# Performance work log

Measured on AMD Instinct MI355X. Metric: run time of the kernel, lower is better.

The kernel has to match this reference:

```python
import jax, jax.numpy as jnp
import numpy as np

B, S, D, E = 4, 2048, 2048, 8


def setup_inputs() -> dict:
    key = jax.random.key(0)
    ks = jax.random.split(key, 5)
    scale = 1.0 / np.sqrt(D)
    x = jax.random.normal(ks[0], (B, S, D), dtype=jnp.float32)
    # experts: torch Linear stores W as [out, in]; y = x @ W.T + b
    expert_w = jax.random.uniform(ks[1], (E, D, D), dtype=jnp.float32, minval=-scale, maxval=scale)
    expert_b = jax.random.uniform(ks[2], (E, D), dtype=jnp.float32, minval=-scale, maxval=scale)
    router_w = jax.random.uniform(ks[3], (E, D), dtype=jnp.float32, minval=-scale, maxval=scale)
    router_b = jax.random.uniform(ks[4], (E,), dtype=jnp.float32, minval=-scale, maxval=scale)
    return {"x": x, "expert_w": expert_w, "expert_b": expert_b,
            "router_w": router_w, "router_b": router_b}


def reference(x, expert_w, expert_b, router_w, router_b):
    b, s, d = x.shape
    n_exp = expert_w.shape[0]
    xf = x.reshape(b * s, d)                       # [N, D]
    logits = xf @ router_w.T + router_b            # [N, E]
    probs = jax.nn.softmax(logits, axis=-1)
    expert_id = jnp.argmax(probs, axis=-1)         # [N] top-1 routing
    top_prob = jnp.max(probs, axis=-1)             # [N] gate weight
    out = jnp.zeros_like(xf)
    # dense-equivalent of the masked gather/scatter: each expert's linear
    # applied to all tokens, masked by routing decision (E is small & static)
    for i in range(n_exp):
        y = xf @ expert_w[i].T + expert_b[i]       # [N, D]
        out = out + jnp.where((expert_id == i)[:, None], y, 0.0)
    out = out * top_prob[:, None]
    # forward never calls compute_loss; returns loss = 0
    return out.reshape(b, s, d), jnp.float32(0.0)
```

## Files before the change

### kernel.cpp

```cpp
#include <hip/hip_runtime.h>
#include <hip/hip_bf16.h>

#define N_TOK 8192
#define DIM   2048
#define NEXP  8
#define BM    288
#define BN    256
#define BK    32
#define NT    (DIM / BK)
#define NBLK  256

#define A_BYTES  (BM * BK * 2)
#define B_BYTES  (BN * BK * 2)
#define RING     (A_BYTES + B_BYTES)
#define DYN_LDS  (4 * RING)

typedef __attribute__((ext_vector_type(8))) short  short8;
typedef __attribute__((ext_vector_type(4))) float  f32x4;
typedef __attribute__((ext_vector_type(4))) unsigned int u32x4;

static __device__ __forceinline__ unsigned int pack_bf2(float a, float b) {
  union { __hip_bfloat16 h; unsigned short u; } ca, cb;
  ca.h = __float2bfloat16(a);
  cb.h = __float2bfloat16(b);
  return ((unsigned int)cb.u << 16) | (unsigned int)ca.u;
}

static __device__ __forceinline__ void gload16(const unsigned short* g, void* l) {
  __builtin_amdgcn_global_load_lds(
      (const __attribute__((address_space(1))) unsigned int*)(const void*)g,
      (__attribute__((address_space(3))) unsigned int*)l, 16, 0, 0);
}

static __device__ __forceinline__ double dot8d(const float4& x0, const float4& x1,
                                               const float4& w0, const float4& w1) {
  double a = 0.0;
  a = fma((double)x0.x, (double)w0.x, a);
  a = fma((double)x0.y, (double)w0.y, a);
  a = fma((double)x0.z, (double)w0.z, a);
  a = fma((double)x0.w, (double)w0.w, a);
  a = fma((double)x1.x, (double)w1.x, a);
  a = fma((double)x1.y, (double)w1.y, a);
  a = fma((double)x1.z, (double)w1.z, a);
  a = fma((double)x1.w, (double)w1.w, a);
  return a;
}

__global__ __launch_bounds__(256) void convw_kernel(
    const float* __restrict__ w, unsigned short* __restrict__ wbuf)
{
  const size_t c0 = (size_t)blockIdx.x * 1024 + threadIdx.x;
  float4 f[8];
#pragma unroll
  for (int i = 0; i < 4; i++) {
    const float4* s = reinterpret_cast<const float4*>(w + (c0 + i * 256) * 8);
    f[2 * i]     = s[0];
    f[2 * i + 1] = s[1];
  }
#pragma unroll
  for (int i = 0; i < 4; i++) {
    u32x4 pk;
    pk[0] = pack_bf2(f[2*i].x,   f[2*i].y);   pk[1] = pack_bf2(f[2*i].z,   f[2*i].w);
    pk[2] = pack_bf2(f[2*i+1].x, f[2*i+1].y); pk[3] = pack_bf2(f[2*i+1].z, f[2*i+1].w);
    *reinterpret_cast<u32x4*>(wbuf + (c0 + i * 256) * 8) = pk;
  }
}

__global__ __launch_bounds__(256, 3) void router_kernel(
    const float* __restrict__ x, const float* __restrict__ rw,
    const float* __restrict__ rb, int* __restrict__ eid,
    float* __restrict__ gate, unsigned short* __restrict__ xb)
{
  const int t    = threadIdx.x;
  const int tok0 = blockIdx.x * 4;

  float4 w0[NEXP], w1[NEXP];
#pragma unroll
  for (int e = 0; e < NEXP; e++) {
    const float4* wr = reinterpret_cast<const float4*>(rw + (size_t)e * DIM);
    w0[e] = wr[2 * t];
    w1[e] = wr[2 * t + 1];
  }
  float4 xv0[4], xv1[4];
#pragma unroll
  for (int k = 0; k < 4; k++) {
    const float4* xr = reinterpret_cast<const float4*>(x + (size_t)(tok0 + k) * DIM);
    xv0[k] = xr[2 * t];
    xv1[k] = xr[2 * t + 1];
  }
#pragma unroll
  for (int k = 0; k < 4; k++) {
    u32x4 pk;
    pk[0] = pack_bf2(xv0[k].x, xv0[k].y); pk[1] = pack_bf2(xv0[k].z, xv0[k].w);
    pk[2] = pack_bf2(xv1[k].x, xv1[k].y); pk[3] = pack_bf2(xv1[k].z, xv1[k].w);
    *reinterpret_cast<u32x4*>(xb + (size_t)(tok0 + k) * DIM + t * 8) = pk;
  }

  __shared__ double red[4][4][NEXP];
  const int lane = t & 63, wv = t >> 6;
#pragma unroll
  for (int k = 0; k < 4; k++) {
    double s[NEXP];
#pragma unroll
    for (int e = 0; e < NEXP; e++) s[e] = dot8d(xv0[k], xv1[k], w0[e], w1[e]);
#pragma unroll
    for (int e = 0; e < NEXP; e++) {
      double v = s[e];
#pragma unroll
      for (int off = 32; off > 0; off >>= 1) v += __shfl_xor(v, off, 64);
      if (lane == 0) red[wv][k][e] = v;
    }
  }
  __syncthreads();
  if (t < 4) {
    double lg[NEXP];
    double lmax = -1e300; int best = 0;
#pragma unroll
    for (int e = 0; e < NEXP; e++) {
      lg[e] = red[0][t][e] + red[1][t][e] + red[2][t][e] + red[3][t][e] + (double)rb[e];
      if (lg[e] > lmax) { lmax = lg[e]; best = e; }
    }
    float den = 0.f;
#pragma unroll
    for (int e = 0; e < NEXP; e++) den += expf((float)(lg[e] - lmax));
    eid[tok0 + t]  = best;
    gate[tok0 + t] = 1.0f / den;
  }
}

__global__ __launch_bounds__(1024) void histo_perm(
    const int* __restrict__ eid, int* __restrict__ counts, int* __restrict__ perm)
{
  __shared__ int hist[NEXP], baseS[NEXP], fillS[NEXP];
  const int t = threadIdx.x;
  if (t < NEXP) { hist[t] = 0; fillS[t] = 0; }
  __syncthreads();
  int my[8];
#pragma unroll
  for (int i = 0; i < 8; i++) {
    my[i] = eid[t + i * 1024];
    atomicAdd(&hist[my[i]], 1);
  }
  __syncthreads();
  if (t == 0) {
    int b = 0;
#pragma unroll
    for (int e = 0; e < NEXP; e++) { counts[e] = hist[e]; baseS[e] = b; b += hist[e]; }
  }
  __syncthreads();
#pragma unroll
  for (int i = 0; i < 8; i++) {
    int pos = baseS[my[i]] + atomicAdd(&fillS[my[i]], 1);
    perm[pos] = t + i * 1024;
  }
}

__global__ __launch_bounds__(512, 2) void moe_gemm(
    const unsigned short* __restrict__ xb, const unsigned short* __restrict__ wb,
    const float* __restrict__ eb, const float* __restrict__ gate,
    const int* __restrict__ perm, const int* __restrict__ counts,
    float* __restrict__ out)
{
  extern __shared__ char smem[];
  __shared__ int   aRowS[BM];
  __shared__ float gateS[BM];

  const int tid  = threadIdx.x;
  const int lane = tid & 63, wid = tid >> 6;

  int ttot = 0;
#pragma unroll
  for (int j = 0; j < NEXP; j++) ttot += (counts[j] + BM - 1) / BM;
  ttot *= 8;
  const int tq = ttot >> 3, tr = ttot & 7;

  const int nA5 = (wid < 2);
  int aR0[3], bR0[2];
  aR0[0] = (wid * 2) * 16;
  aR0[1] = (wid * 2 + 1) * 16;
  aR0[2] = nA5 ? ((16 + wid) * 16) : aR0[0];
  bR0[0] = (wid * 2) * 16;
  bR0[1] = (wid * 2 + 1) * 16;
  int aDst[3], bDst[2];
#pragma unroll
  for (int i = 0; i < 3; i++) aDst[i] = aR0[i] * 64;
#pragma unroll
  for (int i = 0; i < 2; i++) bDst[i] = A_BYTES + bR0[i] * 64;
  const int lrow = lane >> 2;
  const int cblk = (lane & 3) ^ ((lane >> 3) & 3);

  const int l15 = lane & 15;
  const int wr = wid >> 2, wc = wid & 3;
  const int sw   = (((lane >> 4) ^ ((l15 >> 1) & 3)) * 16);
  const int aOff = (wr * 144 + l15) * 64 + sw;
  const int bOff = A_BYTES + (wc * 64 + l15) * 64 + sw;
  const int rsub = (lane >> 4) * 4;

  for (int ti = blockIdx.x; ti < ttot; ti += NBLK) {
    const int k  = ti & 7, j = ti >> 3;
    const int tt = k * tq + (k < tr ? k : tr) + j;
    const int bx = tt >> 3, by = tt & 7;

    int e = 0, rowbase = 0, nrows = 0, found = 0;
    {
      int tsum = 0, bsum = 0;
#pragma unroll
      for (int jj = 0; jj < NEXP; jj++) {
        int cj = counts[jj];
        int te = (cj + BM - 1) / BM;
        if (!found && bx < tsum + te) {
          int loc = bx - tsum;
          e = jj;
          rowbase = bsum + loc * BM;
          int rem = cj - loc * BM;
          nrows = rem < BM ? rem : BM;
          found = 1;
        }
        tsum += te; bsum += cj;
      }
    }

    __syncthreads();
    if (tid < BM) {
      int idx = tid < nrows ? tid : (nrows - 1);
      int tok = perm[rowbase + idx];
      aRowS[tid] = tok;
      gateS[tid] = gate[tok];
    }
    __syncthreads();

    const unsigned short* wB = wb + (size_t)e * DIM * DIM;
    const unsigned short* aSrc[3];
    const unsigned short* bSrc[2];
#pragma unroll
    for (int i = 0; i < 3; i++)
      aSrc[i] = xb + (size_t)aRowS[aR0[i] + lrow] * DIM + cblk * 8;
#pragma unroll
    for (int i = 0; i < 2; i++)
      bSrc[i] = wB + (size_t)(by * BN + bR0[i] + lrow) * DIM + cblk * 8;

#pragma unroll
    for (int p = 0; p < 3; p++) {
      char* base = smem + p * RING;
      gload16(aSrc[0], base + aDst[0]);
      gload16(aSrc[1], base + aDst[1]);
      if (nA5) gload16(aSrc[2], base + aDst[2]);
      gload16(bSrc[0], base + bDst[0]);
      gload16(bSrc[1], base + bDst[1]);
      aSrc[0] += BK; aSrc[1] += BK; aSrc[2] += BK;
      bSrc[0] += BK; bSrc[1] += BK;
    }

    f32x4 acc[9][4] = {};

#pragma unroll 1
    for (int t = 0; t < NT; ++t) {
      if (t < NT - 2) {
        if (nA5) asm volatile("s_waitcnt vmcnt(10)" ::: "memory");
        else     asm volatile("s_waitcnt vmcnt(8)"  ::: "memory");
      } else if (t == NT - 2) {
        if (nA5) asm volatile("s_waitcnt vmcnt(5)" ::: "memory");
        else     asm volatile("s_waitcnt vmcnt(4)" ::: "memory");
      } else {
        asm volatile("s_waitcnt vmcnt(0)" ::: "memory");
      }
      __builtin_amdgcn_s_barrier();

      if (t + 3 < NT) {
        char* base = smem + ((t + 3) & 3) * RING;
        gload16(aSrc[0], base + aDst[0]);
        gload16(aSrc[1], base + aDst[1]);
        if (nA5) gload16(aSrc[2], base + aDst[2]);
        gload16(bSrc[0], base + bDst[0]);
        gload16(bSrc[1], base + bDst[1]);
        aSrc[0] += BK; aSrc[1] += BK; aSrc[2] += BK;
        bSrc[0] += BK; bSrc[1] += BK;
      }

      const char* cur = smem + (t & 3) * RING;
      short8 af[9], bf[4];
#pragma unroll
      for (int n = 0; n < 4; n++) bf[n] = *(const short8*)(cur + bOff + n * 1024);
#pragma unroll
      for (int m = 0; m < 9; m++) af[m] = *(const short8*)(cur + aOff + m * 1024);
      __builtin_amdgcn_s_setprio(1);
#pragma unroll
      for (int m = 0; m < 9; m++)
#pragma unroll
        for (int n = 0; n < 4; n++)
          acc[m][n] = __builtin_amdgcn_mfma_f32_16x16x32_bf16(af[m], bf[n], acc[m][n], 0, 0, 0);
      __builtin_amdgcn_s_setprio(0);
    }

    const int cb = by * BN + wc * 64;
    const float* ebE = eb + (size_t)e * DIM;
    float bias[4];
#pragma unroll
    for (int n = 0; n < 4; n++) bias[n] = ebE[cb + n * 16 + l15];
#pragma unroll
    for (int m = 0; m < 9; m++) {
      int r0 = wr * 144 + m * 16 + rsub;
#pragma unroll
      for (int rg = 0; rg < 4; rg++) {
        int r = r0 + rg;
        if (r < nrows) {
          float g = gateS[r];
          float* orow = out + (size_t)aRowS[r] * DIM + cb;
#pragma unroll
          for (int n = 0; n < 4; n++)
            orow[n * 16 + l15] = (acc[m][n][rg] + bias[n]) * g;
        }
      }
    }
    asm volatile("s_waitcnt vmcnt(0)" ::: "memory");
  }
}

extern "C" void kernel_launch(void* const* d_in, const int* in_sizes, int n_in,
                              void* d_out, int out_size, void* d_ws, size_t ws_size,
                              hipStream_t stream)
{
  const float* x  = (const float*)d_in[0];
  const float* ew = (const float*)d_in[1];
  const float* eb = (const float*)d_in[2];
  const float* rw = (const float*)d_in[3];
  const float* rb = (const float*)d_in[4];
  float* out = (float*)d_out;

  char* ws = (char*)d_ws;
  int*   eid    = (int*)(ws);
  float* gate   = (float*)(ws + 32 * 1024);
  int*   counts = (int*)(ws + 64 * 1024);
  int*   perm   = (int*)(ws + 128 * 1024);
  unsigned short* xbuf = (unsigned short*)(ws + 192 * 1024);
  unsigned short* wbuf = (unsigned short*)(ws + 192 * 1024 + ((size_t)N_TOK * DIM * 2));

  hipFuncSetAttribute(reinterpret_cast<const void*>(moe_gemm),
                      hipFuncAttributeMaxDynamicSharedMemorySize, DYN_LDS);

  hipMemsetAsync(out + (size_t)N_TOK * DIM, 0, sizeof(float), stream);
  convw_kernel<<<4096, 256, 0, stream>>>(ew, wbuf);
  router_kernel<<<N_TOK / 4, 256, 0, stream>>>(x, rw, rb, eid, gate, xbuf);
  histo_perm<<<1, 1024, 0, stream>>>(eid, counts, perm);
  moe_gemm<<<NBLK, 512, DYN_LDS, stream>>>(xbuf, wbuf, eb, gate, perm, counts, out);
}
```

Baseline: 173.1 us.

## Fuse fp32-to-bf16 weight conversion into MoE GEMM B-tile loads

Drops the separate weight conversion kernel and has the GEMM load fp32 expert weights straight into LDS, converting them to bf16 in registers before the MFMAs. This removes a full pass that reads 128MB of fp32 weights and writes bf16 copies. In exchange, B-tile traffic from global memory doubles (fp32), the LDS ring shrinks from 4 to 3 stages, and each k-step adds pack/convert ALU work. Each weight tile is also re-read by many row tiles, so the fp32 reads repeat across blocks.

```diff
diff --git a/kernel.cpp b/kernel.cpp
--- a/kernel.cpp
+++ b/kernel.cpp
@@ -11,9 +11,9 @@
 #define NBLK  256
 
 #define A_BYTES  (BM * BK * 2)
-#define B_BYTES  (BN * BK * 2)
+#define B_BYTES  (BN * BK * 4)
 #define RING     (A_BYTES + B_BYTES)
-#define DYN_LDS  (4 * RING)
+#define DYN_LDS  (3 * RING)
 
 typedef __attribute__((ext_vector_type(8))) short  short8;
 typedef __attribute__((ext_vector_type(4))) float  f32x4;
@@ -26,9 +26,9 @@
   return ((unsigned int)cb.u << 16) | (unsigned int)ca.u;
 }
 
-static __device__ __forceinline__ void gload16(const unsigned short* g, void* l) {
+static __device__ __forceinline__ void gload16(const void* g, void* l) {
   __builtin_amdgcn_global_load_lds(
-      (const __attribute__((address_space(1))) unsigned int*)(const void*)g,
+      (const __attribute__((address_space(1))) unsigned int*)g,
       (__attribute__((address_space(3))) unsigned int*)l, 16, 0, 0);
 }
 
@@ -46,26 +46,6 @@
   return a;
 }
 
-__global__ __launch_bounds__(256) void convw_kernel(
-    const float* __restrict__ w, unsigned short* __restrict__ wbuf)
-{
-  const size_t c0 = (size_t)blockIdx.x * 1024 + threadIdx.x;
-  float4 f[8];
-#pragma unroll
-  for (int i = 0; i < 4; i++) {
-    const float4* s = reinterpret_cast<const float4*>(w + (c0 + i * 256) * 8);
-    f[2 * i]     = s[0];
-    f[2 * i + 1] = s[1];
-  }
-#pragma unroll
-  for (int i = 0; i < 4; i++) {
-    u32x4 pk;
-    pk[0] = pack_bf2(f[2*i].x,   f[2*i].y);   pk[1] = pack_bf2(f[2*i].z,   f[2*i].w);
-    pk[2] = pack_bf2(f[2*i+1].x, f[2*i+1].y); pk[3] = pack_bf2(f[2*i+1].z, f[2*i+1].w);
-    *reinterpret_cast<u32x4*>(wbuf + (c0 + i * 256) * 8) = pk;
-  }
-}
-
 __global__ __launch_bounds__(256, 3) void router_kernel(
     const float* __restrict__ x, const float* __restrict__ rw,
     const float* __restrict__ rb, int* __restrict__ eid,
@@ -156,7 +136,7 @@
 }
 
 __global__ __launch_bounds__(512, 2) void moe_gemm(
-    const unsigned short* __restrict__ xb, const unsigned short* __restrict__ wb,
+    const unsigned short* __restrict__ xb, const float* __restrict__ ew,
     const float* __restrict__ eb, const float* __restrict__ gate,
     const int* __restrict__ perm, const int* __restrict__ counts,
     float* __restrict__ out)
@@ -175,25 +155,36 @@
   const int tq = ttot >> 3, tr = ttot & 7;
 
   const int nA5 = (wid < 2);
-  int aR0[3], bR0[2];
+  int aR0[3];
   aR0[0] = (wid * 2) * 16;
   aR0[1] = (wid * 2 + 1) * 16;
   aR0[2] = nA5 ? ((16 + wid) * 16) : aR0[0];
-  bR0[0] = (wid * 2) * 16;
-  bR0[1] = (wid * 2 + 1) * 16;
-  int aDst[3], bDst[2];
+  int aDst[3];
 #pragma unroll
   for (int i = 0; i < 3; i++) aDst[i] = aR0[i] * 64;
-#pragma unroll
-  for (int i = 0; i < 2; i++) bDst[i] = A_BYTES + bR0[i] * 64;
-  const int lrow = lane >> 2;
-  const int cblk = (lane & 3) ^ ((lane >> 3) & 3);
+  const int lrowA = lane >> 2;
+  const int cblkA = (lane & 3) ^ ((lane >> 3) & 3);
+
+  int bR0[4];
+#pragma unroll
+  for (int i = 0; i < 4; i++) bR0[i] = wid * 32 + i * 8;
+  int bDst[4];
+#pragma unroll
+  for (int i = 0; i < 4; i++) bDst[i] = A_BYTES + bR0[i] * 128;
+  const int lrowB = lane >> 3;
+  const int cblkB = (lane & 7) ^ (lrowB & 7);
 
   const int l15 = lane & 15;
   const int wr = wid >> 2, wc = wid & 3;
-  const int sw   = (((lane >> 4) ^ ((l15 >> 1) & 3)) * 16);
-  const int aOff = (wr * 144 + l15) * 64 + sw;
-  const int bOff = A_BYTES + (wc * 64 + l15) * 64 + sw;
+  const int swA  = (((lane >> 4) ^ ((l15 >> 1) & 3)) * 16);
+  const int aOff = (wr * 144 + l15) * 64 + swA;
+  const int csB  = (lane >> 4) * 2;
+  int bOffN[4];
+#pragma unroll
+  for (int n = 0; n < 4; n++) {
+    int row = wc * 64 + n * 16 + l15;
+    bOffN[n] = A_BYTES + row * 128 + ((csB ^ (row & 7)) << 4);
+  }
   const int rsub = (lane >> 4) * 4;
 
   for (int ti = blockIdx.x; ti < ttot; ti += NBLK) {
@@ -229,60 +220,77 @@
     }
     __syncthreads();
 
-    const unsigned short* wB = wb + (size_t)e * DIM * DIM;
+    const float* wB32 = ew + (size_t)e * DIM * DIM;
     const unsigned short* aSrc[3];
-    const unsigned short* bSrc[2];
+    const float* bSrc[4];
 #pragma unroll
     for (int i = 0; i < 3; i++)
-      aSrc[i] = xb + (size_t)aRowS[aR0[i] + lrow] * DIM + cblk * 8;
-#pragma unroll
-    for (int i = 0; i < 2; i++)
-      bSrc[i] = wB + (size_t)(by * BN + bR0[i] + lrow) * DIM + cblk * 8;
-
-#pragma unroll
-    for (int p = 0; p < 3; p++) {
-      char* base = smem + p * RING;
-      gload16(aSrc[0], base + aDst[0]);
-      gload16(aSrc[1], base + aDst[1]);
-      if (nA5) gload16(aSrc[2], base + aDst[2]);
-      gload16(bSrc[0], base + bDst[0]);
-      gload16(bSrc[1], base + bDst[1]);
-      aSrc[0] += BK; aSrc[1] += BK; aSrc[2] += BK;
-      bSrc[0] += BK; bSrc[1] += BK;
-    }
+      aSrc[i] = xb + (size_t)aRowS[aR0[i] + lrowA] * DIM + cblkA * 8;
+#pragma unroll
+    for (int i = 0; i < 4; i++)
+      bSrc[i] = wB32 + (size_t)(by * BN + bR0[i] + lrowB) * DIM + cblkB * 4;
+
+#define STAGE(SLOTP)                                                        \
+    do {                                                                    \
+      char* sb_ = (SLOTP);                                                  \
+      gload16(aSrc[0], sb_ + aDst[0]);                                      \
+      gload16(aSrc[1], sb_ + aDst[1]);                                      \
+      if (nA5) gload16(aSrc[2], sb_ + aDst[2]);                             \
+      gload16(bSrc[0], sb_ + bDst[0]);                                      \
+      gload16(bSrc[1], sb_ + bDst[1]);                                      \
+      gload16(bSrc[2], sb_ + bDst[2]);                                      \
+      gload16(bSrc[3], sb_ + bDst[3]);                                      \
+      aSrc[0] += BK; aSrc[1] += BK; aSrc[2] += BK;                          \
+      bSrc[0] += BK; bSrc[1] += BK; bSrc[2] += BK; bSrc[3] += BK;           \
+    } while (0)
+
+    STAGE(smem);
+    STAGE(smem + RING);
 
     f32x4 acc[9][4] = {};
 
 #pragma unroll 1
     for (int t = 0; t < NT; ++t) {
-      if (t < NT - 2) {
-        if (nA5) asm volatile("s_waitcnt vmcnt(10)" ::: "memory");
-        else     asm volatile("s_waitcnt vmcnt(8)"  ::: "memory");
-      } else if (t == NT - 2) {
-        if (nA5) asm volatile("s_waitcnt vmcnt(5)" ::: "memory");
-        else     asm volatile("s_waitcnt vmcnt(4)" ::: "memory");
+      if (t < NT - 1) {
+        if (nA5) asm volatile("s_waitcnt vmcnt(7)" ::: "memory");
+        else     asm volatile("s_waitcnt vmcnt(6)" ::: "memory");
       } else {
         asm volatile("s_waitcnt vmcnt(0)" ::: "memory");
       }
       __builtin_amdgcn_s_barrier();
 
-      if (t + 3 < NT) {
-        char* base = smem + ((t + 3) & 3) * RING;
-        gload16(aSrc[0], base + aDst[0]);
-        gload16(aSrc[1], base + aDst[1]);
-        if (nA5) gload16(aSrc[2], base + aDst[2]);
-        gload16(bSrc[0], base + bDst[0]);
-        gload16(bSrc[1], base + bDst[1]);
-        aSrc[0] += BK; aSrc[1] += BK; aSrc[2] += BK;
-        bSrc[0] += BK; bSrc[1] += BK;
-      }
-
-      const char* cur = smem + (t & 3) * RING;
-      short8 af[9], bf[4];
-#pragma unroll
-      for (int n = 0; n < 4; n++) bf[n] = *(const short8*)(cur + bOff + n * 1024);
+      if (t + 2 < NT) {
+        int slot = t + 2;
+        slot -= (slot >= 3) ? 3 : 0;
+        slot -= (slot >= 3) ? 3 : 0;
+        STAGE(smem + (size_t)((t + 2) % 3) * RING);
+        (void)slot;
+      }
+
+      const char* cur = smem + (size_t)(t % 3) * RING;
+
+      f32x4 r0[4], r1[4];
+#pragma unroll
+      for (int n = 0; n < 4; n++) {
+        r0[n] = *(const f32x4*)(cur + bOffN[n]);
+        r1[n] = *(const f32x4*)(cur + (bOffN[n] ^ 16));
+      }
+      short8 bf[4];
+#pragma unroll
+      for (int n = 0; n < 4; n++) {
+        u32x4 pk;
+        pk[0] = pack_bf2(r0[n][0], r0[n][1]);
+        pk[1] = pack_bf2(r0[n][2], r0[n][3]);
+        pk[2] = pack_bf2(r1[n][0], r1[n][1]);
+        pk[3] = pack_bf2(r1[n][2], r1[n][3]);
+        union { u32x4 u; short8 s; } cv;
+        cv.u = pk;
+        bf[n] = cv.s;
+      }
+      short8 af[9];
 #pragma unroll
       for (int m = 0; m < 9; m++) af[m] = *(const short8*)(cur + aOff + m * 1024);
+
       __builtin_amdgcn_s_setprio(1);
 #pragma unroll
       for (int m = 0; m < 9; m++)
@@ -291,6 +299,7 @@
           acc[m][n] = __builtin_amdgcn_mfma_f32_16x16x32_bf16(af[m], bf[n], acc[m][n], 0, 0, 0);
       __builtin_amdgcn_s_setprio(0);
     }
+#undef STAGE
 
     const int cb = by * BN + wc * 64;
     const float* ebE = eb + (size_t)e * DIM;
@@ -299,10 +308,10 @@
     for (int n = 0; n < 4; n++) bias[n] = ebE[cb + n * 16 + l15];
 #pragma unroll
     for (int m = 0; m < 9; m++) {
-      int r0 = wr * 144 + m * 16 + rsub;
+      int r0w = wr * 144 + m * 16 + rsub;
 #pragma unroll
       for (int rg = 0; rg < 4; rg++) {
-        int r = r0 + rg;
+        int r = r0w + rg;
         if (r < nrows) {
           float g = gateS[r];
           float* orow = out + (size_t)aRowS[r] * DIM + cb;
@@ -333,14 +342,12 @@
   int*   counts = (int*)(ws + 64 * 1024);
   int*   perm   = (int*)(ws + 128 * 1024);
   unsigned short* xbuf = (unsigned short*)(ws + 192 * 1024);
-  unsigned short* wbuf = (unsigned short*)(ws + 192 * 1024 + ((size_t)N_TOK * DIM * 2));
 
   hipFuncSetAttribute(reinterpret_cast<const void*>(moe_gemm),
                       hipFuncAttributeMaxDynamicSharedMemorySize, DYN_LDS);
 
   hipMemsetAsync(out + (size_t)N_TOK * DIM, 0, sizeof(float), stream);
-  convw_kernel<<<4096, 256, 0, stream>>>(ew, wbuf);
   router_kernel<<<N_TOK / 4, 256, 0, stream>>>(x, rw, rb, eid, gate, xbuf);
   histo_perm<<<1, 1024, 0, stream>>>(eid, counts, perm);
-  moe_gemm<<<NBLK, 512, DYN_LDS, stream>>>(xbuf, wbuf, eb, gate, perm, counts, out);
-}
+  moe_gemm<<<NBLK, 512, DYN_LDS, stream>>>(xbuf, ew, eb, gate, perm, counts, out);
+}
```

After: 155.3 us. 10.3% less time.
